# Kernel tuning notes

Measured on AMD Instinct MI355X. Metric: run time of the kernel, lower is better.

Reference implementation:

```python
import jax, jax.numpy as jnp
import numpy as np

L, H, D, HS, DFF, V, B, T = 4, 16, 1024, 64, 5120, 32000, 2, 1024
EPS = 1e-5


def setup_inputs() -> dict:
    key = jax.random.key(0)
    ks = iter(jax.random.split(key, 40))
    def nrm(shape):
        return jax.random.normal(next(ks), shape, dtype=jnp.float32) * 0.02
    inp = {}
    inp['idx'] = jax.random.randint(next(ks), (B, T), 0, V)
    inp['tok_emb'] = nrm((V, D))
    inp['pos_emb'] = nrm((T, D))
    for s in ('u', 'm'):  # u = unmasked heads, m = masked (causal) heads
        inp['Wq_' + s] = nrm((L, H, D, HS)); inp['bq_' + s] = jnp.zeros((L, H, HS), jnp.float32)
        inp['Wk_' + s] = nrm((L, H, D, HS)); inp['bk_' + s] = jnp.zeros((L, H, HS), jnp.float32)
        inp['Wv_' + s] = nrm((L, H, D, HS)); inp['bv_' + s] = jnp.zeros((L, H, HS), jnp.float32)
        inp['Wp_' + s] = nrm((L, D, D));     inp['bp_' + s] = jnp.zeros((L, D), jnp.float32)
    inp['W1'] = nrm((L, D, DFF)); inp['b1'] = jnp.zeros((L, DFF), jnp.float32)
    inp['W2'] = nrm((L, DFF, D)); inp['b2'] = jnp.zeros((L, D), jnp.float32)
    ones = jnp.ones((L, D), jnp.float32); zer = jnp.zeros((L, D), jnp.float32)
    inp['lnf_g'] = ones; inp['lnf_b'] = zer     # LayerNorm inside FeedForward
    inp['n1_g'] = ones;  inp['n1_b'] = zer      # Block.norm1
    inp['n2_g'] = ones;  inp['n2_b'] = zer      # Block.norm2
    inp['nf_g'] = jnp.ones((D,), jnp.float32); inp['nf_b'] = jnp.zeros((D,), jnp.float32)
    inp['Wfin'] = nrm((D, V)); inp['bfin'] = jnp.zeros((V,), jnp.float32)
    return inp


def _ln(x, g, b):
    mu = jnp.mean(x, -1, keepdims=True)
    var = jnp.mean((x - mu) ** 2, -1, keepdims=True)
    return (x - mu) / jnp.sqrt(var + EPS) * g + b


def _attn(xn, Wq, bq, Wk, bk, Wv, bv, Wp, bp, causal):
    # xn: [B,T,D]; Wq/Wk/Wv: [H,D,HS] (all heads batched in one einsum)
    q = jnp.einsum('btd,hde->bhte', xn, Wq) + bq[:, None, :]
    k = jnp.einsum('btd,hde->bhte', xn, Wk) + bk[:, None, :]
    v = jnp.einsum('btd,hde->bhte', xn, Wv) + bv[:, None, :]
    w = jnp.einsum('bhte,bhse->bhts', q, k) * (HS ** -0.5)
    if causal:
        mask = jnp.tril(jnp.ones((w.shape[-2], w.shape[-1]), bool))
        w = jnp.where(mask, w, -jnp.inf)
    w = jax.nn.softmax(w, axis=-1)
    o = jnp.einsum('bhts,bhse->bhte', w, v)
    o = o.transpose(0, 2, 1, 3).reshape(xn.shape[0], xn.shape[1], -1)  # concat heads
    return o @ Wp + bp


def _ffn(x, W1, b1, W2, b2, g, b):
    h = jax.nn.leaky_relu(x @ W1 + b1, negative_slope=0.01)
    return _ln(h @ W2 + b2, g, b)


def reference(idx, tok_emb, pos_emb,
              Wq_u, bq_u, Wk_u, bk_u, Wv_u, bv_u, Wp_u, bp_u,
              Wq_m, bq_m, Wk_m, bk_m, Wv_m, bv_m, Wp_m, bp_m,
              W1, b1, W2, b2, lnf_g, lnf_b, n1_g, n1_b, n2_g, n2_b,
              nf_g, nf_b, Wfin, bfin):
    Tn = idx.shape[1]
    x = tok_emb[idx] + pos_emb[:Tn]
    for l in range(L):
        # exact quirky Block wiring from the original code
        x2 = x + _attn(_ln(x, n1_g[l], n1_b[l]), Wq_u[l], bq_u[l], Wk_u[l], bk_u[l],
                       Wv_u[l], bv_u[l], Wp_u[l], bp_u[l], False)
        x = x2 + _ln(_ffn(_ln(x2, n2_g[l], n2_b[l]), W1[l], b1[l], W2[l], b2[l],
                          lnf_g[l], lnf_b[l]), n1_g[l], n1_b[l])
        x2 = x + _attn(_ln(x, n1_g[l], n1_b[l]), Wq_m[l], bq_m[l], Wk_m[l], bk_m[l],
                       Wv_m[l], bv_m[l], Wp_m[l], bp_m[l], True)
        x = x2 + _ln(_ffn(_ln(x2, n2_g[l], n2_b[l]), W1[l], b1[l], W2[l], b2[l],
                          lnf_g[l], lnf_b[l]), n2_g[l], n2_b[l])
    x = _ln(x, nf_g, nf_b)
    return x @ Wfin + bfin  # logits [B,T,V]; targets=None path -> loss is None
```

## Files before the change

kernel.cpp:

```cpp
#include <hip/hip_runtime.h>
#include <hip/hip_bf16.h>
#include <math.h>

#define LNUM 4
#define H 16
#define D 1024
#define HS 64
#define DFF 5120
#define V 32000
#define BB 2
#define T 1024
#define M (BB*T)
#define EPS 1e-5f

typedef __attribute__((ext_vector_type(8))) short bf16x8;
typedef __attribute__((ext_vector_type(4))) float f32x4;

__device__ __forceinline__ void gload16(const void* g, void* l) {
    __builtin_amdgcn_global_load_lds(
        (const __attribute__((address_space(1))) void*)g,
        (__attribute__((address_space(3))) void*)l, 16, 0, 0);
}

__device__ __forceinline__ float wred_sum(float v) {
    #pragma unroll
    for (int off = 32; off; off >>= 1) v += __shfl_xor(v, off, 64);
    return v;
}

__global__ __launch_bounds__(256) void embed_kernel(const int* __restrict__ idx,
        const float* __restrict__ tok, const float* __restrict__ pos,
        float* __restrict__ x) {
    int row = blockIdx.x;
    int t = row & (T - 1);
    int tok_id = idx[row];
    int c = threadIdx.x * 4;
    float4 a = *(const float4*)&tok[(size_t)tok_id * D + c];
    float4 p = *(const float4*)&pos[(size_t)t * D + c];
    a.x += p.x; a.y += p.y; a.z += p.z; a.w += p.w;
    *(float4*)&x[(size_t)row * D + c] = a;
}

__global__ __launch_bounds__(256) void ln_bf16_w4_kernel(const float* __restrict__ in,
        const float* __restrict__ g, const float* __restrict__ b,
        __hip_bfloat16* __restrict__ out) {
    int w = threadIdx.x >> 6, lane = threadIdx.x & 63;
    int row = blockIdx.x * 4 + w;
    const float* rp = in + (size_t)row * D;
    float4 xv[4];
    float s = 0.f;
    #pragma unroll
    for (int c = 0; c < 4; ++c) {
        xv[c] = *(const float4*)&rp[c * 256 + lane * 4];
        s += xv[c].x + xv[c].y + xv[c].z + xv[c].w;
    }
    float mu = wred_sum(s) * (1.0f / D);
    float vs = 0.f;
    #pragma unroll
    for (int c = 0; c < 4; ++c) {
        xv[c].x -= mu; xv[c].y -= mu; xv[c].z -= mu; xv[c].w -= mu;
        vs += xv[c].x*xv[c].x + xv[c].y*xv[c].y + xv[c].z*xv[c].z + xv[c].w*xv[c].w;
    }
    float rs = rsqrtf(wred_sum(vs) * (1.0f / D) + EPS);
    #pragma unroll
    for (int c = 0; c < 4; ++c) {
        int j = c * 256 + lane * 4;
        float4 gv = *(const float4*)&g[j];
        float4 bv = *(const float4*)&b[j];
        union { ushort4 u4; __hip_bfloat16 h[4]; } pk;
        pk.h[0] = __float2bfloat16(xv[c].x * rs * gv.x + bv.x);
        pk.h[1] = __float2bfloat16(xv[c].y * rs * gv.y + bv.y);
        pk.h[2] = __float2bfloat16(xv[c].z * rs * gv.z + bv.z);
        pk.h[3] = __float2bfloat16(xv[c].w * rs * gv.w + bv.w);
        *(ushort4*)&out[(size_t)row * D + j] = pk.u4;
    }
}

template<int NP>
__global__ __launch_bounds__(256) void ffn_tail_kernel(
        const float* __restrict__ part, const float* __restrict__ b2,
        const float* __restrict__ g1, const float* __restrict__ b1,
        const float* __restrict__ g2, const float* __restrict__ b2g,
        const float* __restrict__ res, float* __restrict__ xout,
        const float* __restrict__ gn, const float* __restrict__ bn,
        __hip_bfloat16* __restrict__ xnout) {
    const size_t MD = (size_t)M * D;
    int w = threadIdx.x >> 6, lane = threadIdx.x & 63;
    int row = blockIdx.x * 4 + w;
    size_t ro = (size_t)row * D;
    float4 f[4];
    float s = 0.f;
    #pragma unroll
    for (int c = 0; c < 4; ++c) {
        int j = c * 256 + lane * 4;
        float4 acc = *(const float4*)&b2[j];
        #pragma unroll
        for (int pI = 0; pI < NP; ++pI) {
            float4 pv = *(const float4*)&part[pI * MD + ro + j];
            acc.x += pv.x; acc.y += pv.y; acc.z += pv.z; acc.w += pv.w;
        }
        f[c] = acc;
        s += acc.x + acc.y + acc.z + acc.w;
    }
    float mu = wred_sum(s) * (1.0f / D);
    float vs = 0.f;
    #pragma unroll
    for (int c = 0; c < 4; ++c) {
        f[c].x -= mu; f[c].y -= mu; f[c].z -= mu; f[c].w -= mu;
        vs += f[c].x*f[c].x + f[c].y*f[c].y + f[c].z*f[c].z + f[c].w*f[c].w;
    }
    float rs = rsqrtf(wred_sum(vs) * (1.0f / D) + EPS);
    float s2 = 0.f;
    #pragma unroll
    for (int c = 0; c < 4; ++c) {
        int j = c * 256 + lane * 4;
        float4 gv = *(const float4*)&g1[j];
        float4 bv = *(const float4*)&b1[j];
        f[c].x = f[c].x * rs * gv.x + bv.x;
        f[c].y = f[c].y * rs * gv.y + bv.y;
        f[c].z = f[c].z * rs * gv.z + bv.z;
        f[c].w = f[c].w * rs * gv.w + bv.w;
        s2 += f[c].x + f[c].y + f[c].z + f[c].w;
    }
    float mu2 = wred_sum(s2) * (1.0f / D);
    float vs2 = 0.f;
    #pragma unroll
    for (int c = 0; c < 4; ++c) {
        f[c].x -= mu2; f[c].y -= mu2; f[c].z -= mu2; f[c].w -= mu2;
        vs2 += f[c].x*f[c].x + f[c].y*f[c].y + f[c].z*f[c].z + f[c].w*f[c].w;
    }
    float rs2 = rsqrtf(wred_sum(vs2) * (1.0f / D) + EPS);
    float s3 = 0.f;
    #pragma unroll
    for (int c = 0; c < 4; ++c) {
        int j = c * 256 + lane * 4;
        float4 gv = *(const float4*)&g2[j];
        float4 bv = *(const float4*)&b2g[j];
        float4 rv = *(const float4*)&res[ro + j];
        f[c].x = rv.x + f[c].x * rs2 * gv.x + bv.x;
        f[c].y = rv.y + f[c].y * rs2 * gv.y + bv.y;
        f[c].z = rv.z + f[c].z * rs2 * gv.z + bv.z;
        f[c].w = rv.w + f[c].w * rs2 * gv.w + bv.w;
        *(float4*)&xout[ro + j] = f[c];
        s3 += f[c].x + f[c].y + f[c].z + f[c].w;
    }
    float mu3 = wred_sum(s3) * (1.0f / D);
    float vs3 = 0.f;
    #pragma unroll
    for (int c = 0; c < 4; ++c) {
        f[c].x -= mu3; f[c].y -= mu3; f[c].z -= mu3; f[c].w -= mu3;
        vs3 += f[c].x*f[c].x + f[c].y*f[c].y + f[c].z*f[c].z + f[c].w*f[c].w;
    }
    float rs3 = rsqrtf(wred_sum(vs3) * (1.0f / D) + EPS);
    #pragma unroll
    for (int c = 0; c < 4; ++c) {
        int j = c * 256 + lane * 4;
        float4 gv = *(const float4*)&gn[j];
        float4 bv = *(const float4*)&bn[j];
        union { ushort4 u4; __hip_bfloat16 h[4]; } pk;
        pk.h[0] = __float2bfloat16(f[c].x * rs3 * gv.x + bv.x);
        pk.h[1] = __float2bfloat16(f[c].y * rs3 * gv.y + bv.y);
        pk.h[2] = __float2bfloat16(f[c].z * rs3 * gv.z + bv.z);
        pk.h[3] = __float2bfloat16(f[c].w * rs3 * gv.w + bv.w);
        *(ushort4*)&xnout[ro + j] = pk.u4;
    }
}

__global__ __launch_bounds__(256) void transpose_bf16_kernel(
        const float* __restrict__ in, __hip_bfloat16* __restrict__ out,
        int R, int C, size_t zin, size_t zout) {
    __shared__ float t[32][33];
    in += (size_t)blockIdx.z * zin; out += (size_t)blockIdx.z * zout;
    int tx = threadIdx.x & 31, ty = threadIdx.x >> 5;
    int c0 = blockIdx.x * 32, r0 = blockIdx.y * 32;
    #pragma unroll
    for (int i = 0; i < 4; ++i)
        t[ty + i * 8][tx] = in[(size_t)(r0 + ty + i * 8) * C + c0 + tx];
    __syncthreads();
    #pragma unroll
    for (int i = 0; i < 4; ++i)
        out[(size_t)(c0 + ty + i * 8) * R + r0 + tx] = __float2bfloat16(t[tx][ty + i * 8]);
}

__global__ __launch_bounds__(256) void transpose_qkv_kernel(
        const float* __restrict__ Wq, const float* __restrict__ Wk,
        const float* __restrict__ Wv, short* __restrict__ outT) {
    __shared__ float t[32][33];
    int z = blockIdx.z;
    int which = z >> 4, h = z & 15;
    const float* in = (which == 0 ? Wq : which == 1 ? Wk : Wv) + (size_t)h * D * HS;
    __hip_bfloat16* out = (__hip_bfloat16*)outT + ((size_t)which * H + h) * HS * D;
    int tx = threadIdx.x & 31, ty = threadIdx.x >> 5;
    int c0 = blockIdx.x * 32, r0 = blockIdx.y * 32;
    #pragma unroll
    for (int i = 0; i < 4; ++i)
        t[ty + i * 8][tx] = in[(size_t)(r0 + ty + i * 8) * HS + c0 + tx];
    __syncthreads();
    #pragma unroll
    for (int i = 0; i < 4; ++i)
        out[(size_t)(c0 + ty + i * 8) * D + r0 + tx] = __float2bfloat16(t[tx][ty + i * 8]);
}

__global__ __launch_bounds__(256) void transpose_v_kernel(const short* __restrict__ in,
        short* __restrict__ out) {
    __shared__ short t[32][33];
    int z = blockIdx.z;
    in  += (size_t)z * T * HS;
    out += (size_t)z * HS * T;
    int tx = threadIdx.x & 31, ty = threadIdx.x >> 5;
    int c0 = blockIdx.x * 32, r0 = blockIdx.y * 32;
    #pragma unroll
    for (int i = 0; i < 4; ++i)
        t[ty + i * 8][tx] = in[(size_t)(r0 + ty + i * 8) * HS + c0 + tx];
    __syncthreads();
    #pragma unroll
    for (int i = 0; i < 4; ++i)
        out[(size_t)(c0 + ty + i * 8) * T + r0 + tx] = t[tx][ty + i * 8];
}

template<int BM, int EPI>
__global__ __launch_bounds__(256) void mm_bf16_kernel(
        const short* __restrict__ A, const short* __restrict__ BT,
        const float* __restrict__ bias0, const float* __restrict__ bias1,
        const float* __restrict__ bias2, const float* __restrict__ res,
        float* __restrict__ C0, float* __restrict__ C1, float* __restrict__ C2,
        __hip_bfloat16* __restrict__ Cbf, int N, int Kloop, int lda) {
    constexpr int BK = 32, BN = 128;
    constexpr int MI = BM / 32;
    __shared__ __align__(16) short As[BM * BK];
    __shared__ __align__(16) short Bs[BN * BK];
    int nwg = gridDim.x * gridDim.y;
    int bid = blockIdx.y * gridDim.x + blockIdx.x;
    int bx = blockIdx.x, by = blockIdx.y;
    if (!(nwg & 7)) {
        int s = (bid & 7) * (nwg >> 3) + (bid >> 3);
        bx = s % gridDim.x; by = s / gridDim.x;
    }
    A  += (size_t)blockIdx.z * Kloop;
    BT += (size_t)blockIdx.z * Kloop;
    int tid = threadIdx.x;
    int lane = tid & 63, wid = tid >> 6;
    int wr = wid >> 1, wc = wid & 1;
    int l15 = lane & 15, l16 = lane >> 4;
    int m0 = bx * BM, n0 = by * BN;
    f32x4 acc[MI][4] = {};
    int sr = tid >> 2, sk = (tid & 3) * 8;
    const short* Ag = A + (size_t)(m0 + sr) * lda + sk;
    const short* Bg = BT + (size_t)(n0 + sr) * lda + sk;
    short* Asl = As + tid * 8;
    short* Bsl = Bs + tid * 8;
    for (int k0 = 0; k0 < Kloop; k0 += BK) {
        #pragma unroll
        for (int i = 0; i < BM / 64; ++i)
            gload16(Ag + k0 + (size_t)(i * 64) * lda, Asl + i * 2048);
        #pragma unroll
        for (int i = 0; i < 2; ++i)
            gload16(Bg + k0 + (size_t)(i * 64) * lda, Bsl + i * 2048);
        __syncthreads();
        bf16x8 af[MI], bfv[4];
        const short* Ab = As + (wr * (BM / 2) + l15) * BK + l16 * 8;
        const short* Bb = Bs + (wc * 64 + l15) * BK + l16 * 8;
        #pragma unroll
        for (int mi = 0; mi < MI; ++mi) af[mi] = *(const bf16x8*)(Ab + mi * 16 * BK);
        #pragma unroll
        for (int ni = 0; ni < 4; ++ni) bfv[ni] = *(const bf16x8*)(Bb + ni * 16 * BK);
        __builtin_amdgcn_s_setprio(1);
        #pragma unroll
        for (int mi = 0; mi < MI; ++mi)
            #pragma unroll
            for (int ni = 0; ni < 4; ++ni)
                acc[mi][ni] = __builtin_amdgcn_mfma_f32_16x16x32_bf16(
                    af[mi], bfv[ni], acc[mi][ni], 0, 0, 0);
        __builtin_amdgcn_s_setprio(0);
        __syncthreads();
    }
    int rbase = m0 + wr * (BM / 2) + l16 * 4;
    int cbase = n0 + wc * 64 + l15;
    size_t zoff = (EPI == 4) ? (size_t)blockIdx.z * M * N : 0;
    #pragma unroll
    for (int mi = 0; mi < MI; ++mi) {
        #pragma unroll
        for (int ni = 0; ni < 4; ++ni) {
            int col = cbase + ni * 16;
            float bv = 0.f;
            if (EPI == 3) {
                int z = col >> 10, nn = col & 1023;
                bv = (z == 0 ? bias0 : z == 1 ? bias1 : bias2)[nn];
            } else if (EPI != 4) bv = bias0[col];
            #pragma unroll
            for (int r = 0; r < 4; ++r) {
                int row = rbase + mi * 16 + r;
                float v = acc[mi][ni][r] + bv;
                if (EPI == 0) {
                    C0[(size_t)row * N + col] = v;
                } else if (EPI == 1) {
                    C0[(size_t)row * N + col] = v + res[(size_t)row * N + col];
                } else if (EPI == 2) {
                    v = v > 0.f ? v : 0.01f * v;
                    Cbf[(size_t)row * N + col] = __float2bfloat16(v);
                } else if (EPI == 4) {
                    C0[zoff + (size_t)row * N + col] = v;
                } else {
                    int z = col >> 10;
                    int hh = (col >> 6) & 15, e = col & 63;
                    int b = row >> 10, t = row & (T - 1);
                    __hip_bfloat16* dst = (__hip_bfloat16*)(z == 0 ? C0 : (z == 1 ? C1 : C2));
                    dst[(((size_t)(b * H + hh)) * T + t) * HS + e] = __float2bfloat16(v);
                }
            }
        }
    }
}

template<int CAUSAL>
__global__ __launch_bounds__(256) void attn_mfma_kernel(
        const short* __restrict__ q, const short* __restrict__ k,
        const short* __restrict__ vt, __hip_bfloat16* __restrict__ att) {
    __shared__ __align__(16) short Ks[128 * 64];
    __shared__ __align__(16) short Vs[64 * 128];
    __shared__ __align__(16) short Ps[4][16 * 128];
    int bh = blockIdx.y;
    int bI = bh >> 4, h = bh & 15;
    int tix = blockIdx.x;
    if (CAUSAL) tix = (tix & 1) ? (15 - (tix >> 1)) : (tix >> 1);
    int t0 = tix * 64;
    int tid = threadIdx.x;
    int lane = tid & 63, w = tid >> 6;
    int l15 = lane & 15, l16 = lane >> 4;

    const short* Qg = q + ((size_t)bh * T + t0 + w * 16 + l15) * HS + l16 * 8;
    bf16x8 qf0 = *(const bf16x8*)Qg;
    bf16x8 qf1 = *(const bf16x8*)(Qg + 32);

    const char* Kg = (const char*)(k + (size_t)bh * T * HS);
    const char* Vg = (const char*)(vt + (size_t)bh * HS * T);

    float m_run[4] = {-1e30f, -1e30f, -1e30f, -1e30f};
    float l_run[4] = {0.f, 0.f, 0.f, 0.f};
    f32x4 acc_o[4] = {};
    char* Pw = (char*)Ps[w];
    int pswz = l15 << 4;

    int n_tiles = CAUSAL ? (t0 / 128 + 1) : (T / 128);
    for (int it = 0; it < n_tiles; ++it) {
        int s0 = it * 128;
        __syncthreads();
        #pragma unroll
        for (int i = 0; i < 4; ++i) {
            int o = i * 4096 + tid * 16;
            int row = o >> 7, bir = o & 127;
            gload16(Kg + (size_t)(s0 + row) * 128 + (bir ^ ((row & 7) << 4)),
                    (char*)Ks + o);
        }
        #pragma unroll
        for (int i = 0; i < 4; ++i) {
            int o = i * 4096 + tid * 16;
            int row = o >> 8, bb = o & 255;
            gload16(Vg + (size_t)row * 2048 + s0 * 2 + (bb ^ ((row & 15) << 4)),
                    (char*)Vs + o);
        }
        __syncthreads();

        f32x4 acc_s[8] = {};
        __builtin_amdgcn_s_setprio(1);
        #pragma unroll
        for (int c = 0; c < 8; ++c) {
            int row = c * 16 + l15;
            const char* kb_ = (const char*)Ks + row * 128;
            int swz = (row & 7) << 4;
            bf16x8 kf0 = *(const bf16x8*)(kb_ + ((l16 * 16) ^ swz));
            bf16x8 kf1 = *(const bf16x8*)(kb_ + ((64 + l16 * 16) ^ swz));
            acc_s[c] = __builtin_amdgcn_mfma_f32_16x16x32_bf16(qf0, kf0, acc_s[c], 0, 0, 0);
            acc_s[c] = __builtin_amdgcn_mfma_f32_16x16x32_bf16(qf1, kf1, acc_s[c], 0, 0, 0);
        }
        __builtin_amdgcn_s_setprio(0);

        bool domask = CAUSAL && (it == n_tiles - 1);
        #pragma unroll
        for (int r = 0; r < 4; ++r) {
            float sc[8];
            #pragma unroll
            for (int c = 0; c < 8; ++c) {
                float s = acc_s[c][r];
                if (domask && (s0 + c * 16 + l15) > (t0 + w * 16 + l16 * 4 + r)) s = -1e30f;
                sc[c] = s;
            }
            float tm = fmaxf(fmaxf(fmaxf(sc[0], sc[1]), fmaxf(sc[2], sc[3])),
                             fmaxf(fmaxf(sc[4], sc[5]), fmaxf(sc[6], sc[7])));
            tm = fmaxf(tm, __shfl_xor(tm, 1, 16));
            tm = fmaxf(tm, __shfl_xor(tm, 2, 16));
            tm = fmaxf(tm, __shfl_xor(tm, 4, 16));
            tm = fmaxf(tm, __shfl_xor(tm, 8, 16));
            float mn = fmaxf(m_run[r], tm);
            int prow = l16 * 4 + r;
            int pswzr = prow << 4;
            float ls = 0.f;
            #pragma unroll
            for (int c = 0; c < 8; ++c) {
                float pv = __expf(0.125f * (sc[c] - mn));
                int pbyte = prow * 256 + (((c * 16 + l15) * 2) ^ pswzr);
                *(__hip_bfloat16*)(Pw + pbyte) = __float2bfloat16(pv);
                ls += pv;
            }
            ls += __shfl_xor(ls, 1, 16);
            ls += __shfl_xor(ls, 2, 16);
            ls += __shfl_xor(ls, 4, 16);
            ls += __shfl_xor(ls, 8, 16);
            float alpha = __expf(0.125f * (m_run[r] - mn));
            l_run[r] = l_run[r] * alpha + ls;
            m_run[r] = mn;
            acc_o[0][r] *= alpha; acc_o[1][r] *= alpha;
            acc_o[2][r] *= alpha; acc_o[3][r] *= alpha;
        }

        const char* Pb = Pw + l15 * 256;
        bf16x8 pa[4];
        #pragma unroll
        for (int t = 0; t < 4; ++t)
            pa[t] = *(const bf16x8*)(Pb + ((t * 64 + l16 * 16) ^ pswz));
        __builtin_amdgcn_s_setprio(1);
        #pragma unroll
        for (int ni = 0; ni < 4; ++ni) {
            int row = ni * 16 + l15;
            const char* vb_ = (const char*)Vs + row * 256;
            int swz = (row & 15) << 4;
            #pragma unroll
            for (int t = 0; t < 4; ++t) {
                bf16x8 vf = *(const bf16x8*)(vb_ + ((t * 64 + l16 * 16) ^ swz));
                acc_o[ni] = __builtin_amdgcn_mfma_f32_16x16x32_bf16(pa[t], vf, acc_o[ni], 0, 0, 0);
            }
        }
        __builtin_amdgcn_s_setprio(0);
    }

    float inv[4];
    #pragma unroll
    for (int r = 0; r < 4; ++r) inv[r] = 1.0f / l_run[r];
    #pragma unroll
    for (int ni = 0; ni < 4; ++ni) {
        #pragma unroll
        for (int r = 0; r < 4; ++r) {
            size_t orow = ((size_t)(bI * T) + t0 + w * 16 + l16 * 4 + r) * D
                        + h * HS + ni * 16 + l15;
            att[orow] = __float2bfloat16(acc_o[ni][r] * inv[r]);
        }
    }
}

extern "C" void kernel_launch(void* const* d_in, const int* in_sizes, int n_in,
                              void* d_out, int out_size, void* d_ws, size_t ws_size,
                              hipStream_t stream) {
    const int*   idx     = (const int*)d_in[0];
    const float* tok_emb = (const float*)d_in[1];
    const float* pos_emb = (const float*)d_in[2];
    const float* Wq_u = (const float*)d_in[3],  *bq_u = (const float*)d_in[4];
    const float* Wk_u = (const float*)d_in[5],  *bk_u = (const float*)d_in[6];
    const float* Wv_u = (const float*)d_in[7],  *bv_u = (const float*)d_in[8];
    const float* Wp_u = (const float*)d_in[9],  *bp_u = (const float*)d_in[10];
    const float* Wq_m = (const float*)d_in[11], *bq_m = (const float*)d_in[12];
    const float* Wk_m = (const float*)d_in[13], *bk_m = (const float*)d_in[14];
    const float* Wv_m = (const float*)d_in[15], *bv_m = (const float*)d_in[16];
    const float* Wp_m = (const float*)d_in[17], *bp_m = (const float*)d_in[18];
    const float* W1   = (const float*)d_in[19], *b1   = (const float*)d_in[20];
    const float* W2   = (const float*)d_in[21], *b2   = (const float*)d_in[22];
    const float* lnf_g = (const float*)d_in[23], *lnf_b = (const float*)d_in[24];
    const float* n1_g  = (const float*)d_in[25], *n1_b  = (const float*)d_in[26];
    const float* n2_g  = (const float*)d_in[27], *n2_b  = (const float*)d_in[28];
    const float* nf_g  = (const float*)d_in[29], *nf_b  = (const float*)d_in[30];
    const float* Wfin  = (const float*)d_in[31], *bfin  = (const float*)d_in[32];
    float* out = (float*)d_out;

    char* p = (char*)d_ws;
    auto alloc = [&](size_t bytes) { char* r = p; p += (bytes + 255) & ~255ull; return r; };
    float* x    = (float*)alloc((size_t)M * D * 4);
    float* x2   = (float*)alloc((size_t)M * D * 4);
    float* w2p  = (float*)alloc((size_t)4 * M * D * 4);
    short* qbf  = (short*)alloc((size_t)M * D * 2);
    short* kbf  = (short*)alloc((size_t)M * D * 2);
    short* vbf  = (short*)alloc((size_t)M * D * 2);
    short* vtb  = (short*)alloc((size_t)M * D * 2);
    short* xnb  = (short*)alloc((size_t)M * D * 2);
    short* attb = (short*)alloc((size_t)M * D * 2);
    short* hb   = (short*)alloc((size_t)M * DFF * 2);
    short* WqkvT= (short*)alloc((size_t)3 * 1024 * 1024 * 2);
    short* WpT  = (short*)alloc((size_t)1024 * 1024 * 2);
    short* W1T  = (short*)alloc((size_t)D * DFF * 2);
    short* W2T  = (short*)alloc((size_t)DFF * D * 2);
    short* WfT  = (short*)alloc((size_t)D * V * 2);

    embed_kernel<<<M, 256, 0, stream>>>(idx, tok_emb, pos_emb, x);
    ln_bf16_w4_kernel<<<M / 4, 256, 0, stream>>>(x, n1_g, n1_b, (__hip_bfloat16*)xnb);
    transpose_bf16_kernel<<<dim3(V / 32, D / 32, 1), 256, 0, stream>>>(
        Wfin, (__hip_bfloat16*)WfT, D, V, 0, 0);

    for (int l = 0; l < LNUM; ++l) {
        const float *n1g = n1_g + l * D, *n1b = n1_b + l * D;
        const float *n2g = n2_g + l * D, *n2b = n2_b + l * D;
        const float *lfg = lnf_g + l * D, *lfb = lnf_b + l * D;
        const float *W1l = W1 + (size_t)l * D * DFF, *b1l = b1 + l * DFF;
        const float *W2l = W2 + (size_t)l * DFF * D, *b2l = b2 + l * D;
        transpose_bf16_kernel<<<dim3(DFF / 32, D / 32, 1), 256, 0, stream>>>(
            W1l, (__hip_bfloat16*)W1T, D, DFF, 0, 0);
        transpose_bf16_kernel<<<dim3(D / 32, DFF / 32, 1), 256, 0, stream>>>(
            W2l, (__hip_bfloat16*)W2T, DFF, D, 0, 0);
        for (int half = 0; half < 2; ++half) {
            const float *Wq_, *bq_, *Wk_, *bk_, *Wv_, *bv_, *Wp_, *bp_;
            if (half == 0) { Wq_ = Wq_u; bq_ = bq_u; Wk_ = Wk_u; bk_ = bk_u;
                             Wv_ = Wv_u; bv_ = bv_u; Wp_ = Wp_u; bp_ = bp_u; }
            else           { Wq_ = Wq_m; bq_ = bq_m; Wk_ = Wk_m; bk_ = bk_m;
                             Wv_ = Wv_m; bv_ = bv_m; Wp_ = Wp_m; bp_ = bp_m; }
            Wq_ += (size_t)l * H * D * HS;  bq_ += l * H * HS;
            Wk_ += (size_t)l * H * D * HS;  bk_ += l * H * HS;
            Wv_ += (size_t)l * H * D * HS;  bv_ += l * H * HS;
            Wp_ += (size_t)l * D * D;       bp_ += l * D;

            transpose_qkv_kernel<<<dim3(HS / 32, D / 32, 48), 256, 0, stream>>>(
                Wq_, Wk_, Wv_, WqkvT);
            transpose_bf16_kernel<<<dim3(D / 32, D / 32, 1), 256, 0, stream>>>(
                Wp_, (__hip_bfloat16*)WpT, D, D, 0, 0);

            mm_bf16_kernel<128, 3><<<dim3(M / 128, 3072 / 128), 256, 0, stream>>>(
                xnb, WqkvT, bq_, bk_, bv_, nullptr,
                (float*)qbf, (float*)kbf, (float*)vbf, nullptr, 3072, D, D);
            transpose_v_kernel<<<dim3(HS / 32, T / 32, BB * H), 256, 0, stream>>>(vbf, vtb);
            if (half == 0)
                attn_mfma_kernel<0><<<dim3(T / 64, BB * H), 256, 0, stream>>>(
                    qbf, kbf, vtb, (__hip_bfloat16*)attb);
            else
                attn_mfma_kernel<1><<<dim3(T / 64, BB * H), 256, 0, stream>>>(
                    qbf, kbf, vtb, (__hip_bfloat16*)attb);
            mm_bf16_kernel<64, 1><<<dim3(M / 64, D / 128), 256, 0, stream>>>(
                attb, WpT, bp_, nullptr, nullptr, x, x2, nullptr, nullptr, nullptr, D, D, D);
            ln_bf16_w4_kernel<<<M / 4, 256, 0, stream>>>(x2, n2g, n2b, (__hip_bfloat16*)xnb);
            mm_bf16_kernel<128, 2><<<dim3(M / 128, DFF / 128), 256, 0, stream>>>(
                xnb, W1T, b1l, nullptr, nullptr, nullptr, nullptr, nullptr, nullptr,
                (__hip_bfloat16*)hb, DFF, D, D);
            mm_bf16_kernel<128, 4><<<dim3(M / 128, D / 128, 4), 256, 0, stream>>>(
                hb, W2T, nullptr, nullptr, nullptr, nullptr, w2p, nullptr, nullptr,
                nullptr, D, DFF / 4, DFF);
            const float* og = half ? n2g : n1g;
            const float* ob = half ? n2b : n1b;
            const float* gn; const float* bn;
            if (half == 0)      { gn = n1g; bn = n1b; }
            else if (l < LNUM-1){ gn = n1_g + (l+1)*D; bn = n1_b + (l+1)*D; }
            else                { gn = nf_g; bn = nf_b; }
            ffn_tail_kernel<4><<<M / 4, 256, 0, stream>>>(
                w2p, b2l, lfg, lfb, og, ob, x2, x, gn, bn, (__hip_bfloat16*)xnb);
        }
    }
    mm_bf16_kernel<128, 0><<<dim3(M / 128, V / 128), 256, 0, stream>>>(
        xnb, WfT, bfin, nullptr, nullptr, nullptr, out, nullptr, nullptr, nullptr, V, D, D);
}
```

Measured before the change: 1.707 ms.

## Double-buffer GEMM K tiles with swizzled LDS and BK=64

Rewrites the bf16 GEMM main loop to use two LDS buffers with a prefetch distance of two tiles, issuing global-to-LDS loads for tile t+2 while computing tile t. It controls the wait with explicit vmcnt values. BK is doubled to 64 and the LDS layout is XOR-swizzled by row to avoid bank conflicts on the fragment reads. The aim is to hide global load latency and halve barrier count per K, at the cost of more LDS per block and fragile hand-counted waitcnt values.

Result: faster. 1.650 ms (-3.3%).

```diff
diff --git a/kernel.cpp b/kernel.cpp
--- a/kernel.cpp
+++ b/kernel.cpp
@@ -225,10 +225,10 @@
         const float* __restrict__ bias2, const float* __restrict__ res,
         float* __restrict__ C0, float* __restrict__ C1, float* __restrict__ C2,
         __hip_bfloat16* __restrict__ Cbf, int N, int Kloop, int lda) {
-    constexpr int BK = 32, BN = 128;
+    constexpr int BK = 64, BN = 128;
     constexpr int MI = BM / 32;
-    __shared__ __align__(16) short As[BM * BK];
-    __shared__ __align__(16) short Bs[BN * BK];
+    __shared__ __align__(16) char As[2][BM * 128];
+    __shared__ __align__(16) char Bs[2][BN * 128];
     int nwg = gridDim.x * gridDim.y;
     int bid = blockIdx.y * gridDim.x + blockIdx.x;
     int bx = blockIdx.x, by = blockIdx.y;
@@ -236,44 +236,79 @@
         int s = (bid & 7) * (nwg >> 3) + (bid >> 3);
         bx = s % gridDim.x; by = s / gridDim.x;
     }
-    A  += (size_t)blockIdx.z * Kloop;
-    BT += (size_t)blockIdx.z * Kloop;
     int tid = threadIdx.x;
     int lane = tid & 63, wid = tid >> 6;
     int wr = wid >> 1, wc = wid & 1;
     int l15 = lane & 15, l16 = lane >> 4;
     int m0 = bx * BM, n0 = by * BN;
     f32x4 acc[MI][4] = {};
-    int sr = tid >> 2, sk = (tid & 3) * 8;
-    const short* Ag = A + (size_t)(m0 + sr) * lda + sk;
-    const short* Bg = BT + (size_t)(n0 + sr) * lda + sk;
-    short* Asl = As + tid * 8;
-    short* Bsl = Bs + tid * 8;
-    for (int k0 = 0; k0 < Kloop; k0 += BK) {
-        #pragma unroll
-        for (int i = 0; i < BM / 64; ++i)
-            gload16(Ag + k0 + (size_t)(i * 64) * lda, Asl + i * 2048);
-        #pragma unroll
-        for (int i = 0; i < 2; ++i)
-            gload16(Bg + k0 + (size_t)(i * 64) * lda, Bsl + i * 2048);
-        __syncthreads();
-        bf16x8 af[MI], bfv[4];
-        const short* Ab = As + (wr * (BM / 2) + l15) * BK + l16 * 8;
-        const short* Bb = Bs + (wc * 64 + l15) * BK + l16 * 8;
-        #pragma unroll
-        for (int mi = 0; mi < MI; ++mi) af[mi] = *(const bf16x8*)(Ab + mi * 16 * BK);
-        #pragma unroll
-        for (int ni = 0; ni < 4; ++ni) bfv[ni] = *(const bf16x8*)(Bb + ni * 16 * BK);
-        __builtin_amdgcn_s_setprio(1);
-        #pragma unroll
-        for (int mi = 0; mi < MI; ++mi)
-            #pragma unroll
-            for (int ni = 0; ni < 4; ++ni)
-                acc[mi][ni] = __builtin_amdgcn_mfma_f32_16x16x32_bf16(
-                    af[mi], bfv[ni], acc[mi][ni], 0, 0, 0);
-        __builtin_amdgcn_s_setprio(0);
-        __syncthreads();
-    }
+
+    const size_t lda2 = (size_t)lda * 2;
+    const char* Agc = (const char*)A + (size_t)m0 * lda2 + (size_t)blockIdx.z * Kloop * 2;
+    const char* Bgc = (const char*)BT + (size_t)n0 * lda2 + (size_t)blockIdx.z * Kloop * 2;
+
+    auto stage = [&](int buf, int kbyte) {
+        #pragma unroll
+        for (int i = 0; i < BM / 32; ++i) {
+            int o = i * 4096 + tid * 16;
+            int row = o >> 7, col = o & 127;
+            gload16(Agc + (size_t)row * lda2 + kbyte + (col ^ ((row & 7) << 4)),
+                    As[buf] + o);
+        }
+        #pragma unroll
+        for (int i = 0; i < 4; ++i) {
+            int o = i * 4096 + tid * 16;
+            int row = o >> 7, col = o & 127;
+            gload16(Bgc + (size_t)row * lda2 + kbyte + (col ^ ((row & 7) << 4)),
+                    Bs[buf] + o);
+        }
+    };
+    auto compute = [&](int buf) {
+        #pragma unroll
+        for (int kk = 0; kk < 2; ++kk) {
+            bf16x8 af[MI], bfr[4];
+            #pragma unroll
+            for (int mi = 0; mi < MI; ++mi) {
+                int row = wr * (BM / 2) + mi * 16 + l15;
+                af[mi] = *(const bf16x8*)(As[buf] + row * 128 +
+                          ((kk * 64 + l16 * 16) ^ ((row & 7) << 4)));
+            }
+            #pragma unroll
+            for (int ni = 0; ni < 4; ++ni) {
+                int row = wc * 64 + ni * 16 + l15;
+                bfr[ni] = *(const bf16x8*)(Bs[buf] + row * 128 +
+                          ((kk * 64 + l16 * 16) ^ ((row & 7) << 4)));
+            }
+            __builtin_amdgcn_s_setprio(1);
+            #pragma unroll
+            for (int mi = 0; mi < MI; ++mi)
+                #pragma unroll
+                for (int ni = 0; ni < 4; ++ni)
+                    acc[mi][ni] = __builtin_amdgcn_mfma_f32_16x16x32_bf16(
+                        af[mi], bfr[ni], acc[mi][ni], 0, 0, 0);
+            __builtin_amdgcn_s_setprio(0);
+        }
+    };
+
+    const int NT = Kloop / BK;
+    stage(0, 0);
+    stage(1, 128);
+    for (int t = 0; t < NT; ++t) {
+        if (t < NT - 1) {
+            if constexpr (BM == 128) asm volatile("s_waitcnt vmcnt(8)" ::: "memory");
+            else                     asm volatile("s_waitcnt vmcnt(6)" ::: "memory");
+        } else {
+            asm volatile("s_waitcnt vmcnt(0)" ::: "memory");
+        }
+        __builtin_amdgcn_sched_barrier(0);
+        __builtin_amdgcn_s_barrier();
+        __builtin_amdgcn_sched_barrier(0);
+        compute(t & 1);
+        __builtin_amdgcn_s_barrier();
+        __builtin_amdgcn_sched_barrier(0);
+        if (t + 2 < NT) stage(t & 1, (t + 2) * 128);
+    }
+
     int rbase = m0 + wr * (BM / 2) + l16 * 4;
     int cbase = n0 + wc * 64 + l15;
     size_t zoff = (EPI == 4) ? (size_t)blockIdx.z * M * N : 0;
```
